# Optimization experiments

Hardware: AMD Instinct MI355X
Metric: run time of the kernel (lower is better)

The kernel has to match this reference:

```python
import jax, jax.numpy as jnp
import numpy as np

TEMPERATURE = 0.1

def setup_inputs() -> dict:
    key = jax.random.key(0)
    k1, k2 = jax.random.split(key)
    A = jax.random.normal(k1, (16, 2048, 256), dtype=jnp.float32)
    B = jax.random.normal(k2, (16, 2048, 256), dtype=jnp.float32)
    return {"A": A, "B": B}

def _l2norm(x):
    # F.normalize(p=2, dim=-1): x / max(||x||, eps), eps=1e-12
    n = jnp.sqrt(jnp.sum(x * x, axis=-1, keepdims=True))
    return x / jnp.maximum(n, 1e-12)

def _nce_dir(sim):
    # sim: (B, N, N) logits; labels are the diagonal (row n -> col n)
    # mean over all B*N rows of (logsumexp(row) - row[label])
    lse = jax.nn.logsumexp(sim, axis=-1)            # (B, N)
    diag = jnp.diagonal(sim, axis1=-2, axis2=-1)    # (B, N)
    return jnp.mean(lse - diag)

def reference(A, B):
    emb1 = _l2norm(A)
    emb2 = _l2norm(B)
    sim12 = jnp.einsum("bnc,bmc->bnm", emb1, emb2) / TEMPERATURE  # (B, N, N)
    # sim21 is sim12 transposed per batch; reuse instead of a second bmm
    sim21 = jnp.swapaxes(sim12, -1, -2)
    return _nce_dir(sim12) + _nce_dir(sim21)
```

## Files before the change

kernel.cpp:

```cpp
#include <hip/hip_runtime.h>
#include <hip/hip_bf16.h>

typedef __attribute__((ext_vector_type(8))) __bf16 bf16x8;
typedef __attribute__((ext_vector_type(16))) float f32x16;

#define SCALE_L2E 14.4269504088896f
#define NTOT 32768

#define AS_GLOBAL __attribute__((address_space(1)))
#define AS_LDS    __attribute__((address_space(3)))

__device__ inline void async_copy16(const void* g, void* l) {
    __builtin_amdgcn_global_load_lds((const AS_GLOBAL void*)g, (AS_LDS void*)l, 16, 0, 0);
}

__device__ inline unsigned int f2bf(float f) {
    unsigned int u = __builtin_bit_cast(unsigned int, f);
    u += 0x7fffu + ((u >> 16) & 1u);
    return u >> 16;
}

__device__ inline uint4 pack8(float4 x, float4 y, float s) {
    uint4 r;
    r.x = f2bf(x.x * s) | (f2bf(x.y * s) << 16);
    r.y = f2bf(x.z * s) | (f2bf(x.w * s) << 16);
    r.z = f2bf(y.x * s) | (f2bf(y.y * s) << 16);
    r.w = f2bf(y.z * s) | (f2bf(y.w * s) << 16);
    return r;
}

__device__ inline float dot8(float4 x, float4 y) {
    return x.x*y.x + x.y*y.y + x.z*y.z + x.w*y.w;
}

__global__ __launch_bounds__(256) void nrm_kernel(
        const float* __restrict__ A, const float* __restrict__ B,
        uint4* __restrict__ E1f, uint4* __restrict__ E2f,
        float* __restrict__ diagPart, float* __restrict__ scalars,
        unsigned int* __restrict__ counter) {
    const int tid = threadIdx.x, w = tid >> 6, l = tid & 63;
    const int q = l & 31, h = l >> 5;
    const int wid = blockIdx.x * 4 + w;

    const float4* A4 = (const float4*)A + ((size_t)wid * 8 + h) * 64 + q * 2;
    const float4* B4 = (const float4*)B + ((size_t)wid * 8 + h) * 64 + q * 2;

    float4 a[8], bb[8];
    #pragma unroll
    for (int i = 0; i < 4; ++i) {
        a[2*i]    = A4[i * 128];
        a[2*i+1]  = A4[i * 128 + 1];
        bb[2*i]   = B4[i * 128];
        bb[2*i+1] = B4[i * 128 + 1];
    }

    float ddAcc = 0.f;
    #pragma unroll
    for (int i = 0; i < 4; ++i) {
        float sa = dot8(a[2*i], a[2*i]) + dot8(a[2*i+1], a[2*i+1]);
        float sb = dot8(bb[2*i], bb[2*i]) + dot8(bb[2*i+1], bb[2*i+1]);
        float dd = dot8(a[2*i], bb[2*i]) + dot8(a[2*i+1], bb[2*i+1]);
        #pragma unroll
        for (int off = 1; off <= 16; off <<= 1) {
            sa += __shfl_xor(sa, off);
            sb += __shfl_xor(sb, off);
            dd += __shfl_xor(dd, off);
        }
        const float ia = 1.0f / fmaxf(sqrtf(sa), 1e-12f);
        const float ib = 1.0f / fmaxf(sqrtf(sb), 1e-12f);
        if (q == 0) ddAcc += dd * ia * ib * 10.0f;

        const int n0 = wid * 8 + i * 2 + h;
        const size_t chunk = (size_t)(n0 >> 11) * 65536
                           + (size_t)((n0 & 2047) >> 5) * 1024
                           + (q >> 1) * 64 + (q & 1) * 32 + (n0 & 31);
        E1f[chunk] = pack8(a[2*i], a[2*i+1], ia * SCALE_L2E);
        E2f[chunk] = pack8(bb[2*i], bb[2*i+1], ib);
    }

    #pragma unroll
    for (int off = 1; off <= 32; off <<= 1) ddAcc += __shfl_xor(ddAcc, off);
    __shared__ float part[4];
    if (l == 0) part[w] = ddAcc;
    __syncthreads();
    if (tid == 0) diagPart[blockIdx.x] = part[0] + part[1] + part[2] + part[3];
    if (blockIdx.x == 0 && tid == 0) { scalars[0] = 0.f; *counter = 0u; }
}

__global__ __launch_bounds__(256, 2) void gemm_kernel(
        const bf16x8* __restrict__ E1f, const uint4* __restrict__ E2f,
        float* __restrict__ colPart, float* __restrict__ rowPart) {
    __shared__ bf16x8 Bbuf[2][2048];
    __shared__ float colLDS[2048];

    const int tid = threadIdx.x, w = tid >> 6, l = tid & 63;
    const int b = blockIdx.x & 15;
    const int ct = (blockIdx.x >> 4) & 3, rt = blockIdx.x >> 6;

    for (int i = l; i < 512; i += 64) colLDS[w * 512 + i] = 0.f;

    const uint4* Bb = E2f + (size_t)b * 65536 + (size_t)ct * 16384 + l;

    auto stage = [&](int buf, int sg) {
        const uint4* src = Bb + (size_t)sg * 2048 + (w * 8) * 64;
        #pragma unroll
        for (int j = 0; j < 8; ++j)
            async_copy16(src + j * 64, &Bbuf[buf][(w * 8 + j) * 64]);
    };

    stage(0, 0);

    const bf16x8* Af0 = E1f + (size_t)b * 65536 + (size_t)(rt * 8 + w * 2) * 1024 + l;
    const bf16x8* Af1 = Af0 + 1024;
    bf16x8 af0[16], af1[16];
    #pragma unroll
    for (int kt = 0; kt < 16; ++kt) { af0[kt] = Af0[kt * 64]; af1[kt] = Af1[kt * 64]; }

    float rowAcc0[16], rowAcc1[16];
    #pragma unroll
    for (int r = 0; r < 16; ++r) { rowAcc0[r] = 0.f; rowAcc1[r] = 0.f; }

    auto mmpair = [&](f32x16& x0, f32x16& x1, const bf16x8* Bf) {
        #pragma unroll
        for (int r = 0; r < 16; ++r) { x0[r] = 0.f; x1[r] = 0.f; }
        __builtin_amdgcn_s_setprio(1);
        #pragma unroll
        for (int kt = 0; kt < 16; ++kt) {
            bf16x8 bfrag = Bf[kt * 64];
            x0 = __builtin_amdgcn_mfma_f32_32x32x16_bf16(af0[kt], bfrag, x0, 0, 0, 0);
            x1 = __builtin_amdgcn_mfma_f32_32x32x16_bf16(af1[kt], bfrag, x1, 0, 0, 0);
        }
        __builtin_amdgcn_s_setprio(0);
    };

    auto epi = [&](const f32x16& c, float (&rAcc)[16], int slot) {
        float p = 0.f;
        #pragma unroll
        for (int r = 0; r < 16; ++r) {
            float e = __builtin_amdgcn_exp2f(c[r]);
            rAcc[r] += e;
            p += e;
        }
        p += __shfl_xor(p, 32);
        if (l < 32) colLDS[w * 512 + slot * 32 + l] += p;
    };

    f32x16 c0, c1, d0, d1;
    #pragma unroll
    for (int r = 0; r < 16; ++r) d1[r] = -__builtin_inff();

    __syncthreads();

    for (int sg = 0; sg < 8; ++sg) {
        if (sg < 7) stage((sg + 1) & 1, sg + 1);
        const bf16x8* Bf = Bbuf[sg & 1] + l;

        mmpair(c0, c1, Bf);
        epi(d1, rowAcc1, (sg * 2 - 1) & 15);
        epi(c0, rowAcc0, sg * 2);

        mmpair(d0, d1, Bf + 1024);
        epi(c1, rowAcc1, sg * 2);
        epi(d0, rowAcc0, sg * 2 + 1);

        __syncthreads();
    }
    epi(d1, rowAcc1, 15);

    #pragma unroll
    for (int r = 0; r < 16; ++r) {
        #pragma unroll
        for (int off = 1; off <= 16; off <<= 1) {
            rowAcc0[r] += __shfl_xor(rowAcc0[r], off);
            rowAcc1[r] += __shfl_xor(rowAcc1[r], off);
        }
    }
    if ((l & 31) == 0) {
        float* rs = rowPart + (size_t)(b * 4 + ct) * 2048 + rt * 256 + w * 64 + 4 * (l >> 5);
        #pragma unroll
        for (int r = 0; r < 16; ++r) {
            const int rl = (r & 3) + 8 * (r >> 2);
            rs[rl]      = rowAcc0[r];
            rs[rl + 32] = rowAcc1[r];
        }
    }

    __syncthreads();
    float* gcol = colPart + (size_t)((b * 4 + ct) * 8 + rt) * 512;
    for (int i = tid; i < 512; i += 256)
        gcol[i] = colLDS[i] + colLDS[512 + i] + colLDS[1024 + i] + colLDS[1536 + i];
}

__global__ __launch_bounds__(256) void fin_kernel(
        const float* __restrict__ colPart, const float* __restrict__ rowPart,
        const float* __restrict__ diagPart, float* __restrict__ scalars,
        unsigned int* __restrict__ counter, float* __restrict__ out) {
    const int tid = threadIdx.x;
    float s = 0.f;
    #pragma unroll
    for (int k = 0; k < 2; ++k) {
        const int g = blockIdx.x * 512 + k * 256 + tid;
        const float* cp = colPart + (size_t)(((g >> 11) * 4 + ((g >> 9) & 3)) * 8) * 512 + (g & 511);
        float cs = 0.f;
        #pragma unroll
        for (int rt = 0; rt < 8; ++rt) cs += cp[rt * 512];
        const float* rp = rowPart + (size_t)(g >> 11) * 4 * 2048 + (g & 2047);
        float rsum = rp[0] + rp[2048] + rp[4096] + rp[6144];
        s += logf(cs) + logf(rsum);
    }
    #pragma unroll
    for (int off = 1; off <= 32; off <<= 1) s += __shfl_xor(s, off);
    __shared__ float part[4];
    __shared__ unsigned int lastFlag;
    if ((tid & 63) == 0) part[tid >> 6] = s;
    __syncthreads();
    if (tid == 0) {
        atomicAdd(&scalars[0], part[0] + part[1] + part[2] + part[3]);
        __threadfence();
        lastFlag = (atomicAdd(counter, 1u) == 63u) ? 1u : 0u;
    }
    __syncthreads();
    if (lastFlag) {
        float d = diagPart[tid] + diagPart[tid + 256]
                + diagPart[tid + 512] + diagPart[tid + 768];
        #pragma unroll
        for (int off = 1; off <= 32; off <<= 1) d += __shfl_xor(d, off);
        if ((tid & 63) == 0) part[tid >> 6] = d;
        __syncthreads();
        if (tid == 0) {
            const float diag = part[0] + part[1] + part[2] + part[3];
            const float logSum = atomicAdd(&scalars[0], 0.f);
            out[0] = (logSum - 2.0f * diag) / (float)NTOT;
        }
    }
}

extern "C" void kernel_launch(void* const* d_in, const int* in_sizes, int n_in,
                              void* d_out, int out_size, void* d_ws, size_t ws_size,
                              hipStream_t stream) {
    const float* A = (const float*)d_in[0];
    const float* B = (const float*)d_in[1];

    char* w = (char*)d_ws;
    uint4* E1f = (uint4*)w;
    uint4* E2f = (uint4*)(w + (size_t)16 * 1024 * 1024);
    float* colPart = (float*)(w + (size_t)32 * 1024 * 1024);
    float* rowPart = colPart + 262144;
    float* diagPart = rowPart + 131072;
    float* scalars = diagPart + 1024;
    unsigned int* counter = (unsigned int*)(scalars + 1);

    hipLaunchKernelGGL(nrm_kernel, dim3(1024), dim3(256), 0, stream,
                       A, B, E1f, E2f, diagPart, scalars, counter);
    hipLaunchKernelGGL(gemm_kernel, dim3(512), dim3(256), 0, stream,
                       (const bf16x8*)E1f, (const uint4*)E2f, colPart, rowPart);
    hipLaunchKernelGGL(fin_kernel, dim3(64), dim3(256), 0, stream,
                       colPart, rowPart, diagPart, scalars, counter, (float*)d_out);
}
```

Measured before the change: 152.6 us.

## Split GEMM block into 8 waves each owning one 32-row A tile

The block grows from 4 to 8 waves, and each wave now owns a single 32-row A slice instead of two, with one accumulator chain in place of paired MFMAs. Per-wave register pressure drops (half the A fragments and accumulators) and launch bounds now target more resident waves, aiming to hide latency through occupancy. Staging is spread across 8 waves, and the column partial buffer doubles in LDS. The cost is that each B fragment read from LDS feeds only one MFMA instead of two, which doubles LDS read traffic per FLOP and shortens the independent MFMA chains within each wave.

Result: slower. 251.0 us (+64.4%).

```diff
diff --git a/kernel.cpp b/kernel.cpp
--- a/kernel.cpp
+++ b/kernel.cpp
@@ -87,11 +87,11 @@
     if (blockIdx.x == 0 && tid == 0) { scalars[0] = 0.f; *counter = 0u; }
 }
 
-__global__ __launch_bounds__(256, 2) void gemm_kernel(
+__global__ __launch_bounds__(512, 4) void gemm_kernel(
         const bf16x8* __restrict__ E1f, const uint4* __restrict__ E2f,
         float* __restrict__ colPart, float* __restrict__ rowPart) {
     __shared__ bf16x8 Bbuf[2][2048];
-    __shared__ float colLDS[2048];
+    __shared__ float colLDS[4096];
 
     const int tid = threadIdx.x, w = tid >> 6, l = tid & 63;
     const int b = blockIdx.x & 15;
@@ -102,52 +102,48 @@
     const uint4* Bb = E2f + (size_t)b * 65536 + (size_t)ct * 16384 + l;
 
     auto stage = [&](int buf, int sg) {
-        const uint4* src = Bb + (size_t)sg * 2048 + (w * 8) * 64;
-        #pragma unroll
-        for (int j = 0; j < 8; ++j)
-            async_copy16(src + j * 64, &Bbuf[buf][(w * 8 + j) * 64]);
+        const uint4* src = Bb + (size_t)sg * 2048 + (w * 4) * 64;
+        #pragma unroll
+        for (int j = 0; j < 4; ++j)
+            async_copy16(src + j * 64, &Bbuf[buf][(w * 4 + j) * 64]);
     };
 
     stage(0, 0);
 
-    const bf16x8* Af0 = E1f + (size_t)b * 65536 + (size_t)(rt * 8 + w * 2) * 1024 + l;
-    const bf16x8* Af1 = Af0 + 1024;
-    bf16x8 af0[16], af1[16];
-    #pragma unroll
-    for (int kt = 0; kt < 16; ++kt) { af0[kt] = Af0[kt * 64]; af1[kt] = Af1[kt * 64]; }
-
-    float rowAcc0[16], rowAcc1[16];
-    #pragma unroll
-    for (int r = 0; r < 16; ++r) { rowAcc0[r] = 0.f; rowAcc1[r] = 0.f; }
-
-    auto mmpair = [&](f32x16& x0, f32x16& x1, const bf16x8* Bf) {
-        #pragma unroll
-        for (int r = 0; r < 16; ++r) { x0[r] = 0.f; x1[r] = 0.f; }
+    const bf16x8* Af = E1f + (size_t)b * 65536 + (size_t)(rt * 8 + w) * 1024 + l;
+    bf16x8 af[16];
+    #pragma unroll
+    for (int kt = 0; kt < 16; ++kt) af[kt] = Af[kt * 64];
+
+    float rowAcc[16];
+    #pragma unroll
+    for (int r = 0; r < 16; ++r) rowAcc[r] = 0.f;
+
+    auto chain = [&](f32x16& x, const bf16x8* Bf) {
+        #pragma unroll
+        for (int r = 0; r < 16; ++r) x[r] = 0.f;
         __builtin_amdgcn_s_setprio(1);
         #pragma unroll
-        for (int kt = 0; kt < 16; ++kt) {
-            bf16x8 bfrag = Bf[kt * 64];
-            x0 = __builtin_amdgcn_mfma_f32_32x32x16_bf16(af0[kt], bfrag, x0, 0, 0, 0);
-            x1 = __builtin_amdgcn_mfma_f32_32x32x16_bf16(af1[kt], bfrag, x1, 0, 0, 0);
-        }
+        for (int kt = 0; kt < 16; ++kt)
+            x = __builtin_amdgcn_mfma_f32_32x32x16_bf16(af[kt], Bf[kt * 64], x, 0, 0, 0);
         __builtin_amdgcn_s_setprio(0);
     };
 
-    auto epi = [&](const f32x16& c, float (&rAcc)[16], int slot) {
+    auto epi = [&](const f32x16& c, int slot) {
         float p = 0.f;
         #pragma unroll
         for (int r = 0; r < 16; ++r) {
             float e = __builtin_amdgcn_exp2f(c[r]);
-            rAcc[r] += e;
+            rowAcc[r] += e;
             p += e;
         }
         p += __shfl_xor(p, 32);
         if (l < 32) colLDS[w * 512 + slot * 32 + l] += p;
     };
 
-    f32x16 c0, c1, d0, d1;
-    #pragma unroll
-    for (int r = 0; r < 16; ++r) d1[r] = -__builtin_inff();
+    f32x16 c, d;
+    #pragma unroll
+    for (int r = 0; r < 16; ++r) d[r] = -__builtin_inff();
 
     __syncthreads();
 
@@ -155,40 +151,38 @@
         if (sg < 7) stage((sg + 1) & 1, sg + 1);
         const bf16x8* Bf = Bbuf[sg & 1] + l;
 
-        mmpair(c0, c1, Bf);
-        epi(d1, rowAcc1, (sg * 2 - 1) & 15);
-        epi(c0, rowAcc0, sg * 2);
-
-        mmpair(d0, d1, Bf + 1024);
-        epi(c1, rowAcc1, sg * 2);
-        epi(d0, rowAcc0, sg * 2 + 1);
+        chain(c, Bf);
+        epi(d, (sg * 2 - 1) & 15);
+        chain(d, Bf + 1024);
+        epi(c, sg * 2);
 
         __syncthreads();
     }
-    epi(d1, rowAcc1, 15);
+    epi(d, 15);
 
     #pragma unroll
     for (int r = 0; r < 16; ++r) {
         #pragma unroll
-        for (int off = 1; off <= 16; off <<= 1) {
-            rowAcc0[r] += __shfl_xor(rowAcc0[r], off);
-            rowAcc1[r] += __shfl_xor(rowAcc1[r], off);
-        }
+        for (int off = 1; off <= 16; off <<= 1)
+            rowAcc[r] += __shfl_xor(rowAcc[r], off);
     }
     if ((l & 31) == 0) {
-        float* rs = rowPart + (size_t)(b * 4 + ct) * 2048 + rt * 256 + w * 64 + 4 * (l >> 5);
+        float* rs = rowPart + (size_t)(b * 4 + ct) * 2048 + rt * 256 + w * 32 + 4 * (l >> 5);
         #pragma unroll
         for (int r = 0; r < 16; ++r) {
             const int rl = (r & 3) + 8 * (r >> 2);
-            rs[rl]      = rowAcc0[r];
-            rs[rl + 32] = rowAcc1[r];
+            rs[rl] = rowAcc[r];
         }
     }
 
     __syncthreads();
     float* gcol = colPart + (size_t)((b * 4 + ct) * 8 + rt) * 512;
-    for (int i = tid; i < 512; i += 256)
-        gcol[i] = colLDS[i] + colLDS[512 + i] + colLDS[1024 + i] + colLDS[1536 + i];
+    {
+        float scol = 0.f;
+        #pragma unroll
+        for (int s = 0; s < 8; ++s) scol += colLDS[s * 512 + tid];
+        gcol[tid] = scol;
+    }
 }
 
 __global__ __launch_bounds__(256) void fin_kernel(
@@ -252,7 +246,7 @@
 
     hipLaunchKernelGGL(nrm_kernel, dim3(1024), dim3(256), 0, stream,
                        A, B, E1f, E2f, diagPart, scalars, counter);
-    hipLaunchKernelGGL(gemm_kernel, dim3(512), dim3(256), 0, stream,
+    hipLaunchKernelGGL(gemm_kernel, dim3(512), dim3(512), 0, stream,
                        (const bf16x8*)E1f, (const uint4*)E2f, colPart, rowPart);
     hipLaunchKernelGGL(fin_kernel, dim3(64), dim3(256), 0, stream,
                        colPart, rowPart, diagPart, scalars, counter, (float*)d_out);
```

## Use 512-thread GEMM blocks sharing a quad-buffered B tile across eight waves

Applied to the files above, without the earlier changes.

The similarity GEMM now runs 256 blocks of 8 waves instead of 512 blocks of 4 waves. Each block covers twice as many rows, so every staged B tile in LDS is reused by twice as many waves, halving the B traffic from L2. B staging becomes quad-buffered with a prefetch distance of two stages. Wave halves start on opposite B sub-tiles to spread LDS reads, and the column and row partial layouts shrink to match. In exchange, the old software pipelining that overlapped each tile's exp epilogue with the next MFMA pair is dropped. LDS use grows to about 144 KB per block, so likely only one block fits per CU.

Measured after the change: 190.8 us. 1.25x slower.

```diff
diff --git a/kernel.cpp b/kernel.cpp
--- a/kernel.cpp
+++ b/kernel.cpp
@@ -87,13 +87,14 @@
     if (blockIdx.x == 0 && tid == 0) { scalars[0] = 0.f; *counter = 0u; }
 }
 
-__global__ __launch_bounds__(256, 2) void gemm_kernel(
+__global__ __launch_bounds__(512, 2) void gemm_kernel(
         const bf16x8* __restrict__ E1f, const uint4* __restrict__ E2f,
         float* __restrict__ colPart, float* __restrict__ rowPart) {
-    __shared__ bf16x8 Bbuf[2][2048];
-    __shared__ float colLDS[2048];
+    __shared__ bf16x8 Bbuf[4][2048];
+    __shared__ float colLDS[4096];
 
     const int tid = threadIdx.x, w = tid >> 6, l = tid & 63;
+    const int ho = w >> 2;
     const int b = blockIdx.x & 15;
     const int ct = (blockIdx.x >> 4) & 3, rt = blockIdx.x >> 6;
 
@@ -102,15 +103,16 @@
     const uint4* Bb = E2f + (size_t)b * 65536 + (size_t)ct * 16384 + l;
 
     auto stage = [&](int buf, int sg) {
-        const uint4* src = Bb + (size_t)sg * 2048 + (w * 8) * 64;
-        #pragma unroll
-        for (int j = 0; j < 8; ++j)
-            async_copy16(src + j * 64, &Bbuf[buf][(w * 8 + j) * 64]);
+        const uint4* src = Bb + (size_t)sg * 2048 + (w * 4) * 64;
+        #pragma unroll
+        for (int j = 0; j < 4; ++j)
+            async_copy16(src + j * 64, &Bbuf[buf][(w * 4 + j) * 64]);
     };
 
     stage(0, 0);
-
-    const bf16x8* Af0 = E1f + (size_t)b * 65536 + (size_t)(rt * 8 + w * 2) * 1024 + l;
+    stage(1, 1);
+
+    const bf16x8* Af0 = E1f + (size_t)b * 65536 + (size_t)(rt * 16 + w * 2) * 1024 + l;
     const bf16x8* Af1 = Af0 + 1024;
     bf16x8 af0[16], af1[16];
     #pragma unroll
@@ -145,27 +147,35 @@
         if (l < 32) colLDS[w * 512 + slot * 32 + l] += p;
     };
 
-    f32x16 c0, c1, d0, d1;
-    #pragma unroll
-    for (int r = 0; r < 16; ++r) d1[r] = -__builtin_inff();
-
-    __syncthreads();
-
-    for (int sg = 0; sg < 8; ++sg) {
-        if (sg < 7) stage((sg + 1) & 1, sg + 1);
-        const bf16x8* Bf = Bbuf[sg & 1] + l;
-
-        mmpair(c0, c1, Bf);
-        epi(d1, rowAcc1, (sg * 2 - 1) & 15);
-        epi(c0, rowAcc0, sg * 2);
-
-        mmpair(d0, d1, Bf + 1024);
-        epi(c1, rowAcc1, sg * 2);
-        epi(d0, rowAcc0, sg * 2 + 1);
+    f32x16 c0, c1;
+
+    __syncthreads();
+
+    for (int sgp = 0; sgp < 4; ++sgp) {
+        const int sg0 = sgp * 2, sg1 = sgp * 2 + 1;
+        if (sgp < 3) { stage((sg0 + 2) & 3, sg0 + 2); stage((sg1 + 2) & 3, sg1 + 2); }
+
+        {
+            const bf16x8* Bf = Bbuf[sg0 & 3] + l;
+            mmpair(c0, c1, Bf + ho * 1024);
+            epi(c0, rowAcc0, sg0 * 2 + ho);
+            epi(c1, rowAcc1, sg0 * 2 + ho);
+            mmpair(c0, c1, Bf + (ho ^ 1) * 1024);
+            epi(c0, rowAcc0, sg0 * 2 + (ho ^ 1));
+            epi(c1, rowAcc1, sg0 * 2 + (ho ^ 1));
+        }
+        {
+            const bf16x8* Bf = Bbuf[sg1 & 3] + l;
+            mmpair(c0, c1, Bf + ho * 1024);
+            epi(c0, rowAcc0, sg1 * 2 + ho);
+            epi(c1, rowAcc1, sg1 * 2 + ho);
+            mmpair(c0, c1, Bf + (ho ^ 1) * 1024);
+            epi(c0, rowAcc0, sg1 * 2 + (ho ^ 1));
+            epi(c1, rowAcc1, sg1 * 2 + (ho ^ 1));
+        }
 
         __syncthreads();
     }
-    epi(d1, rowAcc1, 15);
 
     #pragma unroll
     for (int r = 0; r < 16; ++r) {
@@ -176,7 +186,7 @@
         }
     }
     if ((l & 31) == 0) {
-        float* rs = rowPart + (size_t)(b * 4 + ct) * 2048 + rt * 256 + w * 64 + 4 * (l >> 5);
+        float* rs = rowPart + (size_t)(b * 4 + ct) * 2048 + rt * 512 + w * 64 + 4 * (l >> 5);
         #pragma unroll
         for (int r = 0; r < 16; ++r) {
             const int rl = (r & 3) + 8 * (r >> 2);
@@ -186,9 +196,13 @@
     }
 
     __syncthreads();
-    float* gcol = colPart + (size_t)((b * 4 + ct) * 8 + rt) * 512;
-    for (int i = tid; i < 512; i += 256)
-        gcol[i] = colLDS[i] + colLDS[512 + i] + colLDS[1024 + i] + colLDS[1536 + i];
+    float* gcol = colPart + (size_t)((b * 4 + ct) * 4 + rt) * 512;
+    {
+        float scol = 0.f;
+        #pragma unroll
+        for (int s = 0; s < 8; ++s) scol += colLDS[s * 512 + tid];
+        gcol[tid] = scol;
+    }
 }
 
 __global__ __launch_bounds__(256) void fin_kernel(
@@ -200,10 +214,8 @@
     #pragma unroll
     for (int k = 0; k < 2; ++k) {
         const int g = blockIdx.x * 512 + k * 256 + tid;
-        const float* cp = colPart + (size_t)(((g >> 11) * 4 + ((g >> 9) & 3)) * 8) * 512 + (g & 511);
-        float cs = 0.f;
-        #pragma unroll
-        for (int rt = 0; rt < 8; ++rt) cs += cp[rt * 512];
+        const float* cp = colPart + (size_t)(((g >> 11) * 4 + ((g >> 9) & 3)) * 4) * 512 + (g & 511);
+        float cs = cp[0] + cp[512] + cp[1024] + cp[1536];
         const float* rp = rowPart + (size_t)(g >> 11) * 4 * 2048 + (g & 2047);
         float rsum = rp[0] + rp[2048] + rp[4096] + rp[6144];
         s += logf(cs) + logf(rsum);
@@ -245,14 +257,14 @@
     uint4* E1f = (uint4*)w;
     uint4* E2f = (uint4*)(w + (size_t)16 * 1024 * 1024);
     float* colPart = (float*)(w + (size_t)32 * 1024 * 1024);
-    float* rowPart = colPart + 262144;
+    float* rowPart = colPart + 131072;
     float* diagPart = rowPart + 131072;
     float* scalars = diagPart + 1024;
     unsigned int* counter = (unsigned int*)(scalars + 1);
 
     hipLaunchKernelGGL(nrm_kernel, dim3(1024), dim3(256), 0, stream,
                        A, B, E1f, E2f, diagPart, scalars, counter);
-    hipLaunchKernelGGL(gemm_kernel, dim3(512), dim3(256), 0, stream,
+    hipLaunchKernelGGL(gemm_kernel, dim3(256), dim3(512), 0, stream,
                        (const bf16x8*)E1f, (const uint4*)E2f, colPart, rowPart);
     hipLaunchKernelGGL(fin_kernel, dim3(64), dim3(256), 0, stream,
                        colPart, rowPart, diagPart, scalars, counter, (float*)d_out);
```
